# Optimization experiments

Hardware: AMD Instinct MI355X
Metric: run time of the kernel (lower is better)

## Reference

```python
import jax, jax.numpy as jnp
import numpy as np

B, N, D, S, ITERS, EPS = 32, 4096, 512, 8, 3, 1e-8


def layer_norm(x, g, b, eps=1e-5):
    mu = jnp.mean(x, axis=-1, keepdims=True)
    var = jnp.var(x, axis=-1, keepdims=True)
    return (x - mu) * jax.lax.rsqrt(var + eps) * g + b


def setup_inputs() -> dict:
    key = jax.random.key(0)
    ks = jax.random.split(key, 12)
    sc = 1.0 / np.sqrt(D)
    return {
        "inputs": jax.random.normal(ks[0], (B, N, D), jnp.float32),
        "noise": jax.random.normal(ks[1], (B, S, D), jnp.float32),
        "slots_mu": jax.random.normal(ks[2], (1, S, D), jnp.float32),
        "slots_sigma": jnp.ones((1, S, D), jnp.float32),
        "ln_in_g": jnp.ones((D,), jnp.float32), "ln_in_b": jnp.zeros((D,), jnp.float32),
        "ln_s_g": jnp.ones((D,), jnp.float32), "ln_s_b": jnp.zeros((D,), jnp.float32),
        "wq": jax.random.normal(ks[3], (D, D), jnp.float32) * sc,
        "wk": jax.random.normal(ks[4], (D, D), jnp.float32) * sc,
        "wv": jax.random.normal(ks[5], (D, D), jnp.float32) * sc,
        "w_ih": jax.random.normal(ks[6], (3 * D, D), jnp.float32) * sc,
        "w_hh": jax.random.normal(ks[7], (3 * D, D), jnp.float32) * sc,
        "b_ih": jnp.zeros((3 * D,), jnp.float32),
        "b_hh": jnp.zeros((3 * D,), jnp.float32),
        "ln_m_g": jnp.ones((D,), jnp.float32), "ln_m_b": jnp.zeros((D,), jnp.float32),
        "w1": jax.random.normal(ks[8], (D, D), jnp.float32) * sc,
        "b1": jnp.zeros((D,), jnp.float32),
        "w2": jax.random.normal(ks[9], (D, D), jnp.float32) * sc,
        "b2": jnp.zeros((D,), jnp.float32),
    }


def reference(inputs, noise, slots_mu, slots_sigma, ln_in_g, ln_in_b, ln_s_g, ln_s_b,
              wq, wk, wv, w_ih, w_hh, b_ih, b_hh, ln_m_g, ln_m_b, w1, b1, w2, b2):
    # slot init: mu + sigma * N(0,1)
    slots = slots_mu + slots_sigma * noise          # (B,S,D)
    x = layer_norm(inputs, ln_in_g, ln_in_b)        # (B,N,D)
    k = jnp.einsum('bnd,ed->bne', x, wk)            # (B,N,D)
    v = jnp.einsum('bnd,ed->bne', x, wv)            # (B,N,D)
    for _ in range(ITERS):
        slots_prev = slots
        sn = layer_norm(slots, ln_s_g, ln_s_b)
        q = jnp.einsum('bsd,ed->bse', sn, wq)       # (B,S,D)
        logits = jnp.einsum('bnd,bsd->bns', k, q)   # (B,N,S)
        attn = jax.nn.softmax(logits, axis=-1) + EPS  # softmax over slots
        attn = attn / jnp.sum(attn, axis=-1, keepdims=True)
        attn_t = jnp.swapaxes(attn, -1, -2)         # (B,S,N)
        updates = jnp.einsum('bsn,bnd->bsd', attn_t, v)
        # GRUCell(input=updates, hidden=slots_prev)
        gi = jnp.einsum('bsd,ed->bse', updates, w_ih) + b_ih
        gh = jnp.einsum('bsd,ed->bse', slots_prev, w_hh) + b_hh
        gi_r, gi_z, gi_n = jnp.split(gi, 3, axis=-1)
        gh_r, gh_z, gh_n = jnp.split(gh, 3, axis=-1)
        r = jax.nn.sigmoid(gi_r + gh_r)
        z = jax.nn.sigmoid(gi_z + gh_z)
        n = jnp.tanh(gi_n + r * gh_n)
        slots = (1.0 - z) * n + z * slots_prev
        # residual MLP
        h = layer_norm(slots, ln_m_g, ln_m_b)
        h = jax.nn.relu(jnp.einsum('bsd,ed->bse', h, w1) + b1)
        slots = slots + jnp.einsum('bsd,ed->bse', h, w2) + b2
    return slots
```

## Files before the change

kernel.cpp:

```cpp
#include <hip/hip_runtime.h>

#define B_ 32
#define N_ 4096
#define D_ 512
#define S_ 8
#define ITERS_ 3

__device__ __forceinline__ float sigmoid_f(float x) {
    return 1.0f / (1.0f + __expf(-x));
}
__device__ __forceinline__ float tanh_f(float x) {
    float e = __expf(2.0f * x);
    return 1.0f - 2.0f / (e + 1.0f);
}

template<int WT, int LNA>
__device__ void gemm_body(const float* __restrict__ A, const float* __restrict__ W,
                          const float* __restrict__ bias, float* __restrict__ C,
                          int M, int N, int K, int bxi, int byi,
                          const float* __restrict__ stats,
                          const float* __restrict__ lng, const float* __restrict__ lnb,
                          float* smem) {
    float (*As)[68] = (float (*)[68])smem;
    float (*Ws)[36] = (float (*)[36])(smem + 64 * 68);
    int t  = threadIdx.x;
    int bm = byi * 64, bn = bxi * 32;
    int tm = t >> 4, tn = t & 15;
    float acc[4][2] = {{0.f,0.f},{0.f,0.f},{0.f,0.f},{0.f,0.f}};

    for (int kk = 0; kk < K; kk += 64) {
        __syncthreads();
        if (WT == 2) {
#pragma unroll
            for (int r = 0; r < 4; ++r) {
                int idx = t + r * 256;
                int k = idx >> 4, m4 = idx & 15;
                float4 a4 = *(const float4*)(A + (size_t)(kk + k) * M + bm + (m4 << 2));
                *(float4*)&As[k][m4 << 2] = a4;
            }
        } else {
#pragma unroll
            for (int r = 0; r < 4; ++r) {
                int flat = t * 4 + r * 1024;
                int m = flat >> 6, k = flat & 63;
                float4 a4 = *(const float4*)(A + (size_t)(bm + m) * K + kk + k);
                if (LNA) {
                    float mean = stats[(bm + m) * 2];
                    float rs   = stats[(bm + m) * 2 + 1];
                    float4 g4 = *(const float4*)(lng + kk + k);
                    float4 b4 = *(const float4*)(lnb + kk + k);
                    a4.x = fmaf((a4.x - mean) * rs, g4.x, b4.x);
                    a4.y = fmaf((a4.y - mean) * rs, g4.y, b4.y);
                    a4.z = fmaf((a4.z - mean) * rs, g4.z, b4.z);
                    a4.w = fmaf((a4.w - mean) * rs, g4.w, b4.w);
                }
                As[k + 0][m] = a4.x; As[k + 1][m] = a4.y;
                As[k + 2][m] = a4.z; As[k + 3][m] = a4.w;
            }
        }
        if (WT == 1) {
#pragma unroll
            for (int r = 0; r < 2; ++r) {
                int flat = t * 4 + r * 1024;
                int n = flat >> 6, k = flat & 63;
                float4 w4 = *(const float4*)(W + (size_t)(bn + n) * K + kk + k);
                Ws[k + 0][n] = w4.x; Ws[k + 1][n] = w4.y;
                Ws[k + 2][n] = w4.z; Ws[k + 3][n] = w4.w;
            }
        } else {
#pragma unroll
            for (int r = 0; r < 2; ++r) {
                int flat = t * 4 + r * 1024;
                int k = flat >> 5, n = flat & 31;
                float4 w4 = *(const float4*)(W + (size_t)(kk + k) * N + bn + n);
                *(float4*)&Ws[k][n] = w4;
            }
        }
        __syncthreads();
#pragma unroll
        for (int k = 0; k < 64; ++k) {
            float4 a = *(const float4*)&As[k][tm << 2];
            float2 w = *(const float2*)&Ws[k][tn << 1];
            acc[0][0] = fmaf(a.x, w.x, acc[0][0]); acc[0][1] = fmaf(a.x, w.y, acc[0][1]);
            acc[1][0] = fmaf(a.y, w.x, acc[1][0]); acc[1][1] = fmaf(a.y, w.y, acc[1][1]);
            acc[2][0] = fmaf(a.z, w.x, acc[2][0]); acc[2][1] = fmaf(a.z, w.y, acc[2][1]);
            acc[3][0] = fmaf(a.w, w.x, acc[3][0]); acc[3][1] = fmaf(a.w, w.y, acc[3][1]);
        }
    }
#pragma unroll
    for (int i = 0; i < 4; ++i) {
#pragma unroll
        for (int j = 0; j < 2; ++j) {
            int row = bm + (tm << 2) + i;
            int col = bn + (tn << 1) + j;
            float v = acc[i][j];
            if (bias) v += bias[col];
            C[(size_t)row * N + col] = v;
        }
    }
}

__device__ void init_body(const float* __restrict__ noise, const float* __restrict__ mu,
                          const float* __restrict__ sg, float* __restrict__ slots,
                          float* __restrict__ stats, int blk) {
    int wid = threadIdx.x >> 6, lane = threadIdx.x & 63;
    int row = blk * 4 + wid;
    const float4* nz = (const float4*)(noise + (size_t)row * D_);
    const float4* m4 = (const float4*)(mu + (size_t)(row & 7) * D_);
    const float4* s4 = (const float4*)(sg + (size_t)(row & 7) * D_);
    float4 v0 = nz[lane], v1 = nz[64 + lane];
    float4 a0 = m4[lane], a1 = m4[64 + lane];
    float4 c0 = s4[lane], c1 = s4[64 + lane];
    v0.x = fmaf(c0.x, v0.x, a0.x); v0.y = fmaf(c0.y, v0.y, a0.y);
    v0.z = fmaf(c0.z, v0.z, a0.z); v0.w = fmaf(c0.w, v0.w, a0.w);
    v1.x = fmaf(c1.x, v1.x, a1.x); v1.y = fmaf(c1.y, v1.y, a1.y);
    v1.z = fmaf(c1.z, v1.z, a1.z); v1.w = fmaf(c1.w, v1.w, a1.w);
    float4* o4 = (float4*)(slots + (size_t)row * D_);
    o4[lane] = v0; o4[64 + lane] = v1;
    float s1 = v0.x + v0.y + v0.z + v0.w + v1.x + v1.y + v1.z + v1.w;
    float s2 = v0.x*v0.x; s2 = fmaf(v0.y,v0.y,s2); s2 = fmaf(v0.z,v0.z,s2); s2 = fmaf(v0.w,v0.w,s2);
    s2 = fmaf(v1.x,v1.x,s2); s2 = fmaf(v1.y,v1.y,s2); s2 = fmaf(v1.z,v1.z,s2); s2 = fmaf(v1.w,v1.w,s2);
#pragma unroll
    for (int off = 32; off > 0; off >>= 1) {
        s1 += __shfl_xor(s1, off, 64);
        s2 += __shfl_xor(s2, off, 64);
    }
    if (lane == 0) {
        float mean = s1 * (1.0f / D_);
        float var  = s2 * (1.0f / D_) - mean * mean;
        stats[row * 2]     = mean;
        stats[row * 2 + 1] = rsqrtf(var + 1e-5f);
    }
}

__global__ __launch_bounds__(256) void k_pro(const float* __restrict__ wk, const float* __restrict__ wq,
                                             const float* __restrict__ w_ih, const float* __restrict__ wv,
                                             float* __restrict__ Mqk, float* __restrict__ Wiv,
                                             const float* __restrict__ noise, const float* __restrict__ mu,
                                             const float* __restrict__ sg, float* __restrict__ slots,
                                             float* __restrict__ stats) {
    __shared__ float smem[64 * 68 + 64 * 36];
    int blk = blockIdx.x;
    if (blk < 128) {
        gemm_body<2,0>(wk, wq, nullptr, Mqk, 512, 512, 512, blk & 15, blk >> 4,
                       nullptr, nullptr, nullptr, smem);
    } else if (blk < 512) {
        int t2 = blk - 128;
        gemm_body<0,0>(w_ih, wv, nullptr, Wiv, 1536, 512, 512, t2 & 15, t2 >> 4,
                       nullptr, nullptr, nullptr, smem);
    } else {
        init_body(noise, mu, sg, slots, stats, blk - 512);
    }
}

template<int WT, int LNA>
__global__ __launch_bounds__(256) void k_gemm(const float* __restrict__ A, const float* __restrict__ W,
                                              const float* __restrict__ bias, float* __restrict__ C,
                                              int M, int N, int K,
                                              const float* __restrict__ stats,
                                              const float* __restrict__ lng, const float* __restrict__ lnb) {
    __shared__ float smem[64 * 68 + 64 * 36];
    gemm_body<WT,LNA>(A, W, bias, C, M, N, K, blockIdx.x, blockIdx.y, stats, lng, lnb, smem);
}

template<int FIRST>
__global__ __launch_bounds__(512, 1) void k_attn_gh(const float* __restrict__ x,
                                                    const float* __restrict__ qk,
                                                    const float* __restrict__ g,
                                                    const float* __restrict__ bvec,
                                                    float* __restrict__ part,
                                                    float* __restrict__ bsum,
                                                    float2* __restrict__ murs,
                                                    const float* __restrict__ slots,
                                                    const float* __restrict__ w_hh,
                                                    const float* __restrict__ b_hh,
                                                    float* __restrict__ gg) {
    __shared__ float smem[8704];
    const int blk = blockIdx.x;
    const int t = threadIdx.x;

    if (blk < 96) {
        const int ci = blk % 24, ri = blk / 24;
        const int bm = ri * 64, bn = ci * 64;
        float (*As)[68] = (float (*)[68])smem;
        float (*Ws)[68] = (float (*)[68])(smem + 64 * 68);
        const int tm = t >> 5, tn = t & 31;
        float acc[4][2] = {{0.f,0.f},{0.f,0.f},{0.f,0.f},{0.f,0.f}};
        for (int kk = 0; kk < 512; kk += 64) {
            __syncthreads();
#pragma unroll
            for (int r = 0; r < 2; ++r) {
                int flat = t * 4 + r * 2048;
                int m = flat >> 6, k = flat & 63;
                float4 a4 = *(const float4*)(slots + (size_t)(bm + m) * 512 + kk + k);
                As[k + 0][m] = a4.x; As[k + 1][m] = a4.y;
                As[k + 2][m] = a4.z; As[k + 3][m] = a4.w;
            }
#pragma unroll
            for (int r = 0; r < 2; ++r) {
                int flat = t * 4 + r * 2048;
                int n = flat >> 6, k = flat & 63;
                float4 w4 = *(const float4*)(w_hh + (size_t)(bn + n) * 512 + kk + k);
                Ws[k + 0][n] = w4.x; Ws[k + 1][n] = w4.y;
                Ws[k + 2][n] = w4.z; Ws[k + 3][n] = w4.w;
            }
            __syncthreads();
#pragma unroll
            for (int k = 0; k < 64; ++k) {
                const float4 a = *(const float4*)&As[k][tm << 2];
                const float2 w = *(const float2*)&Ws[k][tn << 1];
                acc[0][0] = fmaf(a.x, w.x, acc[0][0]); acc[0][1] = fmaf(a.x, w.y, acc[0][1]);
                acc[1][0] = fmaf(a.y, w.x, acc[1][0]); acc[1][1] = fmaf(a.y, w.y, acc[1][1]);
                acc[2][0] = fmaf(a.z, w.x, acc[2][0]); acc[2][1] = fmaf(a.z, w.y, acc[2][1]);
                acc[3][0] = fmaf(a.w, w.x, acc[3][0]); acc[3][1] = fmaf(a.w, w.y, acc[3][1]);
            }
        }
#pragma unroll
        for (int i = 0; i < 4; ++i) {
#pragma unroll
            for (int j = 0; j < 2; ++j) {
                int row = bm + (tm << 2) + i;
                int col = bn + (tn << 1) + j;
                gg[(size_t)row * 3072 + col] = acc[i][j] + b_hh[col];
            }
        }
        return;
    }

    float* qts  = smem;
    float* dds  = smem + 4096;
    float* wls  = smem + 4480;
    float* mur  = smem + 4864;
    float* redA = smem + 5376;
    float* redB = smem + 5392;
    float* c12  = smem + 5408;
    float* u0s  = smem;
    const int ablk = blk - 96;
    const int nc = ablk & 15, b = ablk >> 4;
    const int w = t >> 6, lane = t & 63;
    const size_t rowbase = (size_t)b * N_ + (size_t)nc * 256;

    {
        const float4* qk4 = (const float4*)(qk + (size_t)b * 4096);
        const float4* g4 = (const float4*)g;
        const float4* b4 = (const float4*)bvec;
        float c1p[2], c2p[2];
#pragma unroll
        for (int r = 0; r < 2; ++r) {
            int f = t + r * 512;
            int k4 = f & 127, sidx = f >> 7;
            float4 v = qk4[f];
            float4 gg4 = g4[k4];
            float4 bb = b4[k4];
            float4 qv = make_float4(v.x*gg4.x, v.y*gg4.y, v.z*gg4.z, v.w*gg4.w);
            *(float4*)&qts[(k4 * 8 + (sidx ^ (k4 & 7))) * 4] = qv;
            c1p[r] = qv.x + qv.y + qv.z + qv.w;
            c2p[r] = bb.x*v.x + bb.y*v.y + bb.z*v.z + bb.w*v.w;
        }
#pragma unroll
        for (int off = 32; off > 0; off >>= 1) {
#pragma unroll
            for (int r = 0; r < 2; ++r) {
                c1p[r] += __shfl_xor(c1p[r], off, 64);
                c2p[r] += __shfl_xor(c2p[r], off, 64);
            }
        }
        if (lane == 0) {
            redA[w * 2 + 0] = c1p[0]; redA[w * 2 + 1] = c1p[1];
            redB[w * 2 + 0] = c2p[0]; redB[w * 2 + 1] = c2p[1];
        }
    }
    if (!FIRST && t < 256) {
        float2 mm = murs[rowbase + t];
        mur[2 * t] = mm.x; mur[2 * t + 1] = mm.y;
    }
    __syncthreads();
    if (t < 8) {
        int s = t;
        float v1, v2;
        if (s < 4) { v1 = redA[4*s]       + redA[4*s + 2];     v2 = redB[4*s]       + redB[4*s + 2]; }
        else       { v1 = redA[4*(s-4)+1] + redA[4*(s-4)+3];   v2 = redB[4*(s-4)+1] + redB[4*(s-4)+3]; }
        c12[s] = v1; c12[8 + s] = v2;
    }
    __syncthreads();

    float4 qa[8], qb[8];
#pragma unroll
    for (int s = 0; s < 8; ++s) {
        qa[s] = *(const float4*)&qts[(lane * 8 + (s ^ (lane & 7))) * 4];
        qb[s] = *(const float4*)&qts[((64 + lane) * 8 + (s ^ (lane & 7))) * 4];
    }

    const bool hb5 = (lane & 32) != 0, hb4 = (lane & 16) != 0, hb3 = (lane & 8) != 0;
    const float cnorm = 1.0f / (1.0f + 8.0f * 1e-8f);
    const float eadd  = 1e-8f * cnorm;

    float4 acc0[8], acc1[8];
#pragma unroll
    for (int s = 0; s < 8; ++s) {
        acc0[s] = make_float4(0.f, 0.f, 0.f, 0.f);
        acc1[s] = make_float4(0.f, 0.f, 0.f, 0.f);
    }
    float aS8[8] = {0,0,0,0,0,0,0,0}, tS8[8] = {0,0,0,0,0,0,0,0};

    const float4* xg = (const float4*)(x + rowbase * D_);
    float4 cur[8], nxt[8];
    {
        int r0 = w * 4;
#pragma unroll
        for (int i = 0; i < 4; ++i) {
            cur[2*i]   = xg[(size_t)(r0 + i) * 128 + lane];
            cur[2*i+1] = xg[(size_t)(r0 + i) * 128 + 64 + lane];
        }
    }

    for (int jb = 0; jb < 8; ++jb) {
#pragma unroll
        for (int i = 0; i < 4; ++i) {
            float4 xa = cur[2*i], xb = cur[2*i+1];
            float dd[8];
#pragma unroll
            for (int s = 0; s < 8; ++s) {
                float td = xa.x * qa[s].x;
                td = fmaf(xa.y, qa[s].y, td); td = fmaf(xa.z, qa[s].z, td); td = fmaf(xa.w, qa[s].w, td);
                td = fmaf(xb.x, qb[s].x, td); td = fmaf(xb.y, qb[s].y, td);
                td = fmaf(xb.z, qb[s].z, td); td = fmaf(xb.w, qb[s].w, td);
                dd[s] = td;
            }
            float r4[4];
#pragma unroll
            for (int s = 0; s < 4; ++s) {
                float snd = hb5 ? dd[s] : dd[s + 4];
                float kp  = hb5 ? dd[s + 4] : dd[s];
                r4[s] = kp + __shfl_xor(snd, 32, 64);
            }
            float r2v[2];
#pragma unroll
            for (int s = 0; s < 2; ++s) {
                float snd = hb4 ? r4[s] : r4[s + 2];
                float kp  = hb4 ? r4[s + 2] : r4[s];
                r2v[s] = kp + __shfl_xor(snd, 16, 64);
            }
            float v;
            {
                float snd = hb3 ? r2v[0] : r2v[1];
                float kp  = hb3 ? r2v[1] : r2v[0];
                v = kp + __shfl_xor(snd, 8, 64);
            }
            v += __shfl_xor(v, 4, 64);
            v += __shfl_xor(v, 2, 64);
            v += __shfl_xor(v, 1, 64);
            int rb = w * 4 + i;
            if ((lane & 7) == 0) dds[rb * 12 + (lane >> 3)] = v;

            if (FIRST) {
                float sx = xa.x + xa.y + xa.z + xa.w + xb.x + xb.y + xb.z + xb.w;
                float sxx = xa.x*xa.x; sxx = fmaf(xa.y,xa.y,sxx); sxx = fmaf(xa.z,xa.z,sxx); sxx = fmaf(xa.w,xa.w,sxx);
                sxx = fmaf(xb.x,xb.x,sxx); sxx = fmaf(xb.y,xb.y,sxx); sxx = fmaf(xb.z,xb.z,sxx); sxx = fmaf(xb.w,xb.w,sxx);
#pragma unroll
                for (int off = 32; off > 0; off >>= 1) {
                    sx  += __shfl_xor(sx, off, 64);
                    sxx += __shfl_xor(sxx, off, 64);
                }
                float mean = sx * (1.0f / D_);
                float rs   = rsqrtf(sxx * (1.0f / D_) - mean * mean + 1e-5f);
                if (lane == 0) {
                    int br = jb * 32 + rb;
                    mur[br * 2] = mean; mur[br * 2 + 1] = rs;
                    murs[rowbase + br] = make_float2(mean, rs);
                }
            }
        }
        __syncthreads();
        if (w == 0 && lane < 32) {
            int br = jb * 32 + lane;
            float4 d03 = *(const float4*)&dds[lane * 12];
            float4 d47 = *(const float4*)&dds[lane * 12 + 4];
            float mean = mur[br * 2], rs = mur[br * 2 + 1];
            float mc = -rs * mean;
            float lg[8];
            lg[0] = fmaf(rs, d03.x, fmaf(mc, c12[0], c12[8]));
            lg[1] = fmaf(rs, d03.y, fmaf(mc, c12[1], c12[9]));
            lg[2] = fmaf(rs, d03.z, fmaf(mc, c12[2], c12[10]));
            lg[3] = fmaf(rs, d03.w, fmaf(mc, c12[3], c12[11]));
            lg[4] = fmaf(rs, d47.x, fmaf(mc, c12[4], c12[12]));
            lg[5] = fmaf(rs, d47.y, fmaf(mc, c12[5], c12[13]));
            lg[6] = fmaf(rs, d47.z, fmaf(mc, c12[6], c12[14]));
            lg[7] = fmaf(rs, d47.w, fmaf(mc, c12[7], c12[15]));
            float mx = lg[0];
#pragma unroll
            for (int s = 1; s < 8; ++s) mx = fmaxf(mx, lg[s]);
            float p[8], psum = 0.f;
#pragma unroll
            for (int s = 0; s < 8; ++s) { p[s] = __expf(lg[s] - mx); psum += p[s]; }
            float ip = cnorm / psum;
            float wv[8];
#pragma unroll
            for (int s = 0; s < 8; ++s) {
                float a = fmaf(p[s], ip, eadd);
                wv[s] = a * rs;
                aS8[s] += a;
                tS8[s] = fmaf(wv[s], mean, tS8[s]);
            }
            *(float4*)&wls[lane * 12]     = make_float4(wv[0], wv[1], wv[2], wv[3]);
            *(float4*)&wls[lane * 12 + 4] = make_float4(wv[4], wv[5], wv[6], wv[7]);
        }
        __syncthreads();
        {
            int jn = (jb < 7) ? jb + 1 : 7;
            int r0 = jn * 32 + w * 4;
#pragma unroll
            for (int i = 0; i < 4; ++i) {
                nxt[2*i]   = xg[(size_t)(r0 + i) * 128 + lane];
                nxt[2*i+1] = xg[(size_t)(r0 + i) * 128 + 64 + lane];
            }
        }
#pragma unroll
        for (int i = 0; i < 4; ++i) {
            int rb = w * 4 + i;
            float4 w03 = *(const float4*)&wls[rb * 12];
            float4 w47 = *(const float4*)&wls[rb * 12 + 4];
            float4 xa = cur[2*i], xb = cur[2*i+1];
            acc0[0].x = fmaf(w03.x, xa.x, acc0[0].x); acc0[0].y = fmaf(w03.x, xa.y, acc0[0].y);
            acc0[0].z = fmaf(w03.x, xa.z, acc0[0].z); acc0[0].w = fmaf(w03.x, xa.w, acc0[0].w);
            acc1[0].x = fmaf(w03.x, xb.x, acc1[0].x); acc1[0].y = fmaf(w03.x, xb.y, acc1[0].y);
            acc1[0].z = fmaf(w03.x, xb.z, acc1[0].z); acc1[0].w = fmaf(w03.x, xb.w, acc1[0].w);
            acc0[1].x = fmaf(w03.y, xa.x, acc0[1].x); acc0[1].y = fmaf(w03.y, xa.y, acc0[1].y);
            acc0[1].z = fmaf(w03.y, xa.z, acc0[1].z); acc0[1].w = fmaf(w03.y, xa.w, acc0[1].w);
            acc1[1].x = fmaf(w03.y, xb.x, acc1[1].x); acc1[1].y = fmaf(w03.y, xb.y, acc1[1].y);
            acc1[1].z = fmaf(w03.y, xb.z, acc1[1].z); acc1[1].w = fmaf(w03.y, xb.w, acc1[1].w);
            acc0[2].x = fmaf(w03.z, xa.x, acc0[2].x); acc0[2].y = fmaf(w03.z, xa.y, acc0[2].y);
            acc0[2].z = fmaf(w03.z, xa.z, acc0[2].z); acc0[2].w = fmaf(w03.z, xa.w, acc0[2].w);
            acc1[2].x = fmaf(w03.z, xb.x, acc1[2].x); acc1[2].y = fmaf(w03.z, xb.y, acc1[2].y);
            acc1[2].z = fmaf(w03.z, xb.z, acc1[2].z); acc1[2].w = fmaf(w03.z, xb.w, acc1[2].w);
            acc0[3].x = fmaf(w03.w, xa.x, acc0[3].x); acc0[3].y = fmaf(w03.w, xa.y, acc0[3].y);
            acc0[3].z = fmaf(w03.w, xa.z, acc0[3].z); acc0[3].w = fmaf(w03.w, xa.w, acc0[3].w);
            acc1[3].x = fmaf(w03.w, xb.x, acc1[3].x); acc1[3].y = fmaf(w03.w, xb.y, acc1[3].y);
            acc1[3].z = fmaf(w03.w, xb.z, acc1[3].z); acc1[3].w = fmaf(w03.w, xb.w, acc1[3].w);
            acc0[4].x = fmaf(w47.x, xa.x, acc0[4].x); acc0[4].y = fmaf(w47.x, xa.y, acc0[4].y);
            acc0[4].z = fmaf(w47.x, xa.z, acc0[4].z); acc0[4].w = fmaf(w47.x, xa.w, acc0[4].w);
            acc1[4].x = fmaf(w47.x, xb.x, acc1[4].x); acc1[4].y = fmaf(w47.x, xb.y, acc1[4].y);
            acc1[4].z = fmaf(w47.x, xb.z, acc1[4].z); acc1[4].w = fmaf(w47.x, xb.w, acc1[4].w);
            acc0[5].x = fmaf(w47.y, xa.x, acc0[5].x); acc0[5].y = fmaf(w47.y, xa.y, acc0[5].y);
            acc0[5].z = fmaf(w47.y, xa.z, acc0[5].z); acc0[5].w = fmaf(w47.y, xa.w, acc0[5].w);
            acc1[5].x = fmaf(w47.y, xb.x, acc1[5].x); acc1[5].y = fmaf(w47.y, xb.y, acc1[5].y);
            acc1[5].z = fmaf(w47.y, xb.z, acc1[5].z); acc1[5].w = fmaf(w47.y, xb.w, acc1[5].w);
            acc0[6].x = fmaf(w47.z, xa.x, acc0[6].x); acc0[6].y = fmaf(w47.z, xa.y, acc0[6].y);
            acc0[6].z = fmaf(w47.z, xa.z, acc0[6].z); acc0[6].w = fmaf(w47.z, xa.w, acc0[6].w);
            acc1[6].x = fmaf(w47.z, xb.x, acc1[6].x); acc1[6].y = fmaf(w47.z, xb.y, acc1[6].y);
            acc1[6].z = fmaf(w47.z, xb.z, acc1[6].z); acc1[6].w = fmaf(w47.z, xb.w, acc1[6].w);
            acc0[7].x = fmaf(w47.w, xa.x, acc0[7].x); acc0[7].y = fmaf(w47.w, xa.y, acc0[7].y);
            acc0[7].z = fmaf(w47.w, xa.z, acc0[7].z); acc0[7].w = fmaf(w47.w, xa.w, acc0[7].w);
            acc1[7].x = fmaf(w47.w, xb.x, acc1[7].x); acc1[7].y = fmaf(w47.w, xb.y, acc1[7].y);
            acc1[7].z = fmaf(w47.w, xb.z, acc1[7].z); acc1[7].w = fmaf(w47.w, xb.w, acc1[7].w);
        }
#pragma unroll
        for (int i = 0; i < 8; ++i) cur[i] = nxt[i];
        __syncthreads();
    }

    if (w == 0) {
#pragma unroll
        for (int off = 32; off > 0; off >>= 1) {
#pragma unroll
            for (int s = 0; s < 8; ++s) {
                aS8[s] += __shfl_xor(aS8[s], off, 64);
                tS8[s] += __shfl_xor(tS8[s], off, 64);
            }
        }
        if (lane == 0) {
            float* bs = bsum + (size_t)(b * 16 + nc) * 16;
#pragma unroll
            for (int s = 0; s < 8; ++s) { bs[s] = aS8[s]; bs[8 + s] = tS8[s]; }
        }
    }
    for (int w2 = 0; w2 < 8; ++w2) {
        if (w == w2) {
#pragma unroll
            for (int s = 0; s < 8; ++s) {
                float* p0 = &u0s[s * 512 + (lane << 2)];
                float* p1 = p0 + 256;
                if (w2 == 0) {
                    *(float4*)p0 = acc0[s];
                    *(float4*)p1 = acc1[s];
                } else {
                    float4 v0 = *(float4*)p0;
                    v0.x += acc0[s].x; v0.y += acc0[s].y; v0.z += acc0[s].z; v0.w += acc0[s].w;
                    *(float4*)p0 = v0;
                    float4 v1 = *(float4*)p1;
                    v1.x += acc1[s].x; v1.y += acc1[s].y; v1.z += acc1[s].z; v1.w += acc1[s].w;
                    *(float4*)p1 = v1;
                }
            }
        }
        __syncthreads();
    }
    float4* d4 = (float4*)(part + (size_t)(b * 16 + nc) * 4096);
    const float4* s4 = (const float4*)u0s;
    d4[t] = s4[t];
    d4[t + 512] = s4[t + 512];
}

__global__ __launch_bounds__(512) void k_ured(const float* __restrict__ part,
                                              const float* __restrict__ bsum,
                                              const float* __restrict__ g,
                                              const float* __restrict__ bvec,
                                              float* __restrict__ u0) {
    const int bs = blockIdx.x;
    const int b = bs >> 3, s = bs & 7;
    const int d = threadIdx.x;
    float Av = 0.f, Tv = 0.f;
#pragma unroll
    for (int nc = 0; nc < 16; ++nc) {
        Av += bsum[(size_t)(b * 16 + nc) * 16 + s];
        Tv += bsum[(size_t)(b * 16 + nc) * 16 + 8 + s];
    }
    float p = 0.f;
#pragma unroll
    for (int nc = 0; nc < 16; ++nc)
        p += part[(size_t)(b * 16 + nc) * 4096 + s * 512 + d];
    u0[(size_t)bs * 512 + d] = fmaf(g[d], p - Tv, Av * bvec[d]);
}

__global__ __launch_bounds__(256) void k_gi(const float* __restrict__ u0,
                                            const float* __restrict__ Wiv,
                                            const float* __restrict__ b_ih,
                                            float* __restrict__ gg) {
    __shared__ float As[64][68];
    __shared__ float Ws[64][36];
    const int t = threadIdx.x;
    const int bn = blockIdx.x * 32;
    const int bm = blockIdx.y * 64;
    int tm = t >> 4, tn = t & 15;
    float acc[4][2] = {{0.f,0.f},{0.f,0.f},{0.f,0.f},{0.f,0.f}};

    for (int kk = 0; kk < 512; kk += 64) {
        __syncthreads();
#pragma unroll
        for (int r = 0; r < 4; ++r) {
            int flat = t * 4 + r * 1024;
            int m = flat >> 6, k = flat & 63;
            float4 a4 = *(const float4*)(u0 + (size_t)(bm + m) * 512 + kk + k);
            As[k + 0][m] = a4.x; As[k + 1][m] = a4.y;
            As[k + 2][m] = a4.z; As[k + 3][m] = a4.w;
        }
#pragma unroll
        for (int r = 0; r < 2; ++r) {
            int flat = t * 4 + r * 1024;
            int n = flat >> 6, k = flat & 63;
            float4 w4 = *(const float4*)(Wiv + (size_t)(bn + n) * 512 + kk + k);
            Ws[k + 0][n] = w4.x; Ws[k + 1][n] = w4.y;
            Ws[k + 2][n] = w4.z; Ws[k + 3][n] = w4.w;
        }
        __syncthreads();
#pragma unroll
        for (int k = 0; k < 64; ++k) {
            float4 a = *(const float4*)&As[k][tm << 2];
            float2 w = *(const float2*)&Ws[k][tn << 1];
            acc[0][0] = fmaf(a.x, w.x, acc[0][0]); acc[0][1] = fmaf(a.x, w.y, acc[0][1]);
            acc[1][0] = fmaf(a.y, w.x, acc[1][0]); acc[1][1] = fmaf(a.y, w.y, acc[1][1]);
            acc[2][0] = fmaf(a.z, w.x, acc[2][0]); acc[2][1] = fmaf(a.z, w.y, acc[2][1]);
            acc[3][0] = fmaf(a.w, w.x, acc[3][0]); acc[3][1] = fmaf(a.w, w.y, acc[3][1]);
        }
    }
#pragma unroll
    for (int i = 0; i < 4; ++i) {
#pragma unroll
        for (int j = 0; j < 2; ++j) {
            int row = bm + (tm << 2) + i;
            int cw  = bn + (tn << 1) + j;
            gg[(size_t)row * 3072 + 1536 + cw] = acc[i][j] + b_ih[cw];
        }
    }
}

__global__ __launch_bounds__(512) void k_p2(const float* __restrict__ gg,
                                            const float* __restrict__ slots,
                                            const float* __restrict__ w1, const float* __restrict__ b1,
                                            const float* __restrict__ w2, const float* __restrict__ b2,
                                            const float* __restrict__ wqkT,
                                            const float* __restrict__ ln_m_g, const float* __restrict__ ln_m_b,
                                            const float* __restrict__ ln_s_g, const float* __restrict__ ln_s_b,
                                            float* __restrict__ dst, float* __restrict__ qkout, int last) {
    __shared__ float s2s[2][512];
    __shared__ float t0s[2][512];
    __shared__ float hs[2][512];
    __shared__ float stat[4];
    const int t = threadIdx.x;
    const int wid = t >> 6, lane = t & 63;
    const int r0 = blockIdx.x * 2;

#pragma unroll
    for (int j = 0; j < 2; ++j) {
        int flat = t + j * 512;
        int r = flat >> 9, d = flat & 511;
        size_t row = r0 + r;
        const float* ghb = gg + row * 3072;
        const float* gib = ghb + 1536;
        float gir = gib[d], giz = gib[d + 512], gin = gib[d + 1024];
        float ghr = ghb[d], ghz = ghb[d + 512], ghn = ghb[d + 1024];
        float rr = sigmoid_f(gir + ghr);
        float zz = sigmoid_f(giz + ghz);
        float nn = tanh_f(fmaf(rr, ghn, gin));
        float sp = slots[row * 512 + d];
        s2s[r][d] = fmaf(1.0f - zz, nn, zz * sp);
    }
    __syncthreads();
    if (wid < 2) {
        const float4* sr = (const float4*)s2s[wid];
        float4 a = sr[lane], bq = sr[64 + lane];
        float s1 = a.x + a.y + a.z + a.w + bq.x + bq.y + bq.z + bq.w;
        float s2 = a.x*a.x; s2 = fmaf(a.y,a.y,s2); s2 = fmaf(a.z,a.z,s2); s2 = fmaf(a.w,a.w,s2);
        s2 = fmaf(bq.x,bq.x,s2); s2 = fmaf(bq.y,bq.y,s2); s2 = fmaf(bq.z,bq.z,s2); s2 = fmaf(bq.w,bq.w,s2);
#pragma unroll
        for (int off = 32; off > 0; off >>= 1) {
            s1 += __shfl_xor(s1, off, 64);
            s2 += __shfl_xor(s2, off, 64);
        }
        if (lane == 0) {
            float mean = s1 * (1.0f / D_);
            float var  = s2 * (1.0f / D_) - mean * mean;
            stat[wid * 2] = mean;
            stat[wid * 2 + 1] = rsqrtf(var + 1e-5f);
        }
    }
    __syncthreads();
#pragma unroll
    for (int j = 0; j < 2; ++j) {
        int flat = t + j * 512;
        int r = flat >> 9, d = flat & 511;
        t0s[r][d] = fmaf((s2s[r][d] - stat[r * 2]) * stat[r * 2 + 1], ln_m_g[d], ln_m_b[d]);
    }
    __syncthreads();
    {
        const int c = t;
        const float4* wr = (const float4*)(w1 + (size_t)c * 512);
        float a0 = 0.f, a1 = 0.f;
#pragma unroll 8
        for (int k4 = 0; k4 < 128; ++k4) {
            float4 w4 = wr[k4];
            float4 q0 = *(const float4*)&t0s[0][k4 << 2];
            float4 q1 = *(const float4*)&t0s[1][k4 << 2];
            a0 = fmaf(q0.x, w4.x, a0); a0 = fmaf(q0.y, w4.y, a0);
            a0 = fmaf(q0.z, w4.z, a0); a0 = fmaf(q0.w, w4.w, a0);
            a1 = fmaf(q1.x, w4.x, a1); a1 = fmaf(q1.y, w4.y, a1);
            a1 = fmaf(q1.z, w4.z, a1); a1 = fmaf(q1.w, w4.w, a1);
        }
        float bc = b1[c];
        hs[0][c] = fmaxf(a0 + bc, 0.f);
        hs[1][c] = fmaxf(a1 + bc, 0.f);
    }
    __syncthreads();
    {
        const int c = t;
        const float4* wr = (const float4*)(w2 + (size_t)c * 512);
        float a0 = 0.f, a1 = 0.f;
#pragma unroll 8
        for (int k4 = 0; k4 < 128; ++k4) {
            float4 w4 = wr[k4];
            float4 q0 = *(const float4*)&hs[0][k4 << 2];
            float4 q1 = *(const float4*)&hs[1][k4 << 2];
            a0 = fmaf(q0.x, w4.x, a0); a0 = fmaf(q0.y, w4.y, a0);
            a0 = fmaf(q0.z, w4.z, a0); a0 = fmaf(q0.w, w4.w, a0);
            a1 = fmaf(q1.x, w4.x, a1); a1 = fmaf(q1.y, w4.y, a1);
            a1 = fmaf(q1.z, w4.z, a1); a1 = fmaf(q1.w, w4.w, a1);
        }
        float bc = b2[c];
        float o0 = s2s[0][c] + a0 + bc;
        float o1 = s2s[1][c] + a1 + bc;
        dst[(size_t)r0 * 512 + c] = o0;
        dst[(size_t)(r0 + 1) * 512 + c] = o1;
        s2s[0][c] = o0;
        s2s[1][c] = o1;
    }
    if (last) return;
    __syncthreads();
    if (wid < 2) {
        const float4* sr = (const float4*)s2s[wid];
        float4 a = sr[lane], bq = sr[64 + lane];
        float s1 = a.x + a.y + a.z + a.w + bq.x + bq.y + bq.z + bq.w;
        float s2 = a.x*a.x; s2 = fmaf(a.y,a.y,s2); s2 = fmaf(a.z,a.z,s2); s2 = fmaf(a.w,a.w,s2);
        s2 = fmaf(bq.x,bq.x,s2); s2 = fmaf(bq.y,bq.y,s2); s2 = fmaf(bq.z,bq.z,s2); s2 = fmaf(bq.w,bq.w,s2);
#pragma unroll
        for (int off = 32; off > 0; off >>= 1) {
            s1 += __shfl_xor(s1, off, 64);
            s2 += __shfl_xor(s2, off, 64);
        }
        if (lane == 0) {
            float mean = s1 * (1.0f / D_);
            float var  = s2 * (1.0f / D_) - mean * mean;
            stat[wid * 2] = mean;
            stat[wid * 2 + 1] = rsqrtf(var + 1e-5f);
        }
    }
    __syncthreads();
#pragma unroll
    for (int j = 0; j < 2; ++j) {
        int flat = t + j * 512;
        int r = flat >> 9, d = flat & 511;
        t0s[r][d] = fmaf((s2s[r][d] - stat[r * 2]) * stat[r * 2 + 1], ln_s_g[d], ln_s_b[d]);
    }
    __syncthreads();
    {
        const int c = t;
        const float4* wr = (const float4*)(wqkT + (size_t)c * 512);
        float a0 = 0.f, a1 = 0.f;
#pragma unroll 8
        for (int k4 = 0; k4 < 128; ++k4) {
            float4 w4 = wr[k4];
            float4 q0 = *(const float4*)&t0s[0][k4 << 2];
            float4 q1 = *(const float4*)&t0s[1][k4 << 2];
            a0 = fmaf(q0.x, w4.x, a0); a0 = fmaf(q0.y, w4.y, a0);
            a0 = fmaf(q0.z, w4.z, a0); a0 = fmaf(q0.w, w4.w, a0);
            a1 = fmaf(q1.x, w4.x, a1); a1 = fmaf(q1.y, w4.y, a1);
            a1 = fmaf(q1.z, w4.z, a1); a1 = fmaf(q1.w, w4.w, a1);
        }
        qkout[(size_t)r0 * 512 + c] = a0;
        qkout[(size_t)(r0 + 1) * 512 + c] = a1;
    }
}

extern "C" void kernel_launch(void* const* d_in, const int* in_sizes, int n_in,
                              void* d_out, int out_size, void* d_ws, size_t ws_size,
                              hipStream_t stream) {
    const float* inputs  = (const float*)d_in[0];
    const float* noise   = (const float*)d_in[1];
    const float* mu      = (const float*)d_in[2];
    const float* sg      = (const float*)d_in[3];
    const float* ln_in_g = (const float*)d_in[4];
    const float* ln_in_b = (const float*)d_in[5];
    const float* ln_s_g  = (const float*)d_in[6];
    const float* ln_s_b  = (const float*)d_in[7];
    const float* wq      = (const float*)d_in[8];
    const float* wk      = (const float*)d_in[9];
    const float* wv      = (const float*)d_in[10];
    const float* w_ih    = (const float*)d_in[11];
    const float* w_hh    = (const float*)d_in[12];
    const float* b_ih    = (const float*)d_in[13];
    const float* b_hh    = (const float*)d_in[14];
    const float* ln_m_g  = (const float*)d_in[15];
    const float* ln_m_b  = (const float*)d_in[16];
    const float* w1      = (const float*)d_in[17];
    const float* b1      = (const float*)d_in[18];
    const float* w2      = (const float*)d_in[19];
    const float* b2      = (const float*)d_in[20];

    float* ws = (float*)d_ws;
    const size_t SLOT = (size_t)B_ * S_ * D_;
    size_t o = 0;
    float* slots = ws + o; o += SLOT;
    float* qk    = ws + o; o += SLOT;
    float* u0    = ws + o; o += SLOT;
    float* gg    = ws + o; o += (size_t)256 * 3072;
    float* Mqk   = ws + o; o += (size_t)D_ * D_;
    float* Wiv   = ws + o; o += (size_t)3 * D_ * D_;
    float* statsS= ws + o; o += 512;
    float* part  = ws + o; o += (size_t)16 * B_ * 4096;
    float* bsum  = ws + o; o += (size_t)B_ * 16 * 16;
    float2* murs = (float2*)(ws + o); o += (size_t)2 * B_ * N_;

    k_pro<<<576, 256, 0, stream>>>(wk, wq, w_ih, wv, Mqk, Wiv, noise, mu, sg, slots, statsS);
    k_gemm<1,1><<<dim3(16, 4), 256, 0, stream>>>(slots, Mqk, nullptr, qk,
                                                 256, 512, 512, statsS, ln_s_g, ln_s_b);

    for (int it = 0; it < ITERS_; ++it) {
        if (it == 0)
            k_attn_gh<1><<<608, 512, 0, stream>>>(inputs, qk, ln_in_g, ln_in_b, part, bsum,
                                                  murs, slots, w_hh, b_hh, gg);
        else
            k_attn_gh<0><<<608, 512, 0, stream>>>(inputs, qk, ln_in_g, ln_in_b, part, bsum,
                                                  murs, slots, w_hh, b_hh, gg);
        k_ured<<<256, 512, 0, stream>>>(part, bsum, ln_in_g, ln_in_b, u0);
        k_gi<<<dim3(48, 4), 256, 0, stream>>>(u0, Wiv, b_ih, gg);
        int last = (it == ITERS_ - 1);
        float* dst = last ? (float*)d_out : slots;
        k_p2<<<128, 512, 0, stream>>>(gg, slots, w1, b1, w2, b2, Mqk,
                                      ln_m_g, ln_m_b, ln_s_g, ln_s_b, dst, qk, last);
    }
}
```

Before: 677.0 us.

## Double attention rows per block and distribute softmax per wave to drop barriers

Each attention block now covers 512 rows instead of 256, halving the number of attention blocks and the partial buffers that k_ured must reduce. The per-chunk softmax is computed by four lanes in each wave for that wave's own rows instead of by wave 0 after a block barrier, which removes two __syncthreads per chunk. The prefetch of the next x chunk moves to the top of the loop. Per-block slot sums are reduced through shared memory across waves. In exchange, fewer blocks may lower occupancy and load balance across CUs, and the shared-memory layout changes.

```diff
diff --git a/kernel.cpp b/kernel.cpp
--- a/kernel.cpp
+++ b/kernel.cpp
@@ -231,14 +231,14 @@
     float* dds  = smem + 4096;
     float* wls  = smem + 4480;
     float* mur  = smem + 4864;
-    float* redA = smem + 5376;
-    float* redB = smem + 5392;
-    float* c12  = smem + 5408;
+    float* redA = smem + 5888;
+    float* redB = smem + 5952;
+    float* c12  = smem + 6016;
     float* u0s  = smem;
     const int ablk = blk - 96;
-    const int nc = ablk & 15, b = ablk >> 4;
+    const int nc = ablk & 7, b = ablk >> 3;
     const int w = t >> 6, lane = t & 63;
-    const size_t rowbase = (size_t)b * N_ + (size_t)nc * 256;
+    const size_t rowbase = (size_t)b * N_ + (size_t)nc * 512;
 
     {
         const float4* qk4 = (const float4*)(qk + (size_t)b * 4096);
@@ -270,7 +270,7 @@
             redB[w * 2 + 0] = c2p[0]; redB[w * 2 + 1] = c2p[1];
         }
     }
-    if (!FIRST && t < 256) {
+    if (!FIRST) {
         float2 mm = murs[rowbase + t];
         mur[2 * t] = mm.x; mur[2 * t + 1] = mm.y;
     }
@@ -314,7 +314,16 @@
         }
     }
 
-    for (int jb = 0; jb < 8; ++jb) {
+    for (int jb = 0; jb < 16; ++jb) {
+        {
+            int jn = (jb < 15) ? jb + 1 : 15;
+            int r0 = jn * 32 + w * 4;
+#pragma unroll
+            for (int i = 0; i < 4; ++i) {
+                nxt[2*i]   = xg[(size_t)(r0 + i) * 128 + lane];
+                nxt[2*i+1] = xg[(size_t)(r0 + i) * 128 + 64 + lane];
+            }
+        }
 #pragma unroll
         for (int i = 0; i < 4; ++i) {
             float4 xa = cur[2*i], xb = cur[2*i+1];
@@ -371,11 +380,11 @@
                 }
             }
         }
-        __syncthreads();
-        if (w == 0 && lane < 32) {
-            int br = jb * 32 + lane;
-            float4 d03 = *(const float4*)&dds[lane * 12];
-            float4 d47 = *(const float4*)&dds[lane * 12 + 4];
+        if (lane < 4) {
+            int rb = w * 4 + lane;
+            int br = jb * 32 + rb;
+            float4 d03 = *(const float4*)&dds[rb * 12];
+            float4 d47 = *(const float4*)&dds[rb * 12 + 4];
             float mean = mur[br * 2], rs = mur[br * 2 + 1];
             float mc = -rs * mean;
             float lg[8];
@@ -402,18 +411,8 @@
                 aS8[s] += a;
                 tS8[s] = fmaf(wv[s], mean, tS8[s]);
             }
-            *(float4*)&wls[lane * 12]     = make_float4(wv[0], wv[1], wv[2], wv[3]);
-            *(float4*)&wls[lane * 12 + 4] = make_float4(wv[4], wv[5], wv[6], wv[7]);
-        }
-        __syncthreads();
-        {
-            int jn = (jb < 7) ? jb + 1 : 7;
-            int r0 = jn * 32 + w * 4;
-#pragma unroll
-            for (int i = 0; i < 4; ++i) {
-                nxt[2*i]   = xg[(size_t)(r0 + i) * 128 + lane];
-                nxt[2*i+1] = xg[(size_t)(r0 + i) * 128 + 64 + lane];
-            }
+            *(float4*)&wls[rb * 12]     = make_float4(wv[0], wv[1], wv[2], wv[3]);
+            *(float4*)&wls[rb * 12 + 4] = make_float4(wv[4], wv[5], wv[6], wv[7]);
         }
 #pragma unroll
         for (int i = 0; i < 4; ++i) {
@@ -456,23 +455,18 @@
         }
 #pragma unroll
         for (int i = 0; i < 8; ++i) cur[i] = nxt[i];
-        __syncthreads();
-    }
-
-    if (w == 0) {
-#pragma unroll
-        for (int off = 32; off > 0; off >>= 1) {
-#pragma unroll
-            for (int s = 0; s < 8; ++s) {
-                aS8[s] += __shfl_xor(aS8[s], off, 64);
-                tS8[s] += __shfl_xor(tS8[s], off, 64);
-            }
-        }
-        if (lane == 0) {
-            float* bs = bsum + (size_t)(b * 16 + nc) * 16;
-#pragma unroll
-            for (int s = 0; s < 8; ++s) { bs[s] = aS8[s]; bs[8 + s] = tS8[s]; }
-        }
+    }
+
+#pragma unroll
+    for (int s = 0; s < 8; ++s) {
+        aS8[s] += __shfl_xor(aS8[s], 1, 64);
+        aS8[s] += __shfl_xor(aS8[s], 2, 64);
+        tS8[s] += __shfl_xor(tS8[s], 1, 64);
+        tS8[s] += __shfl_xor(tS8[s], 2, 64);
+    }
+    if (lane == 0) {
+#pragma unroll
+        for (int s = 0; s < 8; ++s) { redA[w * 8 + s] = aS8[s]; redB[w * 8 + s] = tS8[s]; }
     }
     for (int w2 = 0; w2 < 8; ++w2) {
         if (w == w2) {
@@ -495,7 +489,15 @@
         }
         __syncthreads();
     }
-    float4* d4 = (float4*)(part + (size_t)(b * 16 + nc) * 4096);
+    if (t < 16) {
+        int s = t & 7;
+        const float* src = (t < 8) ? redA : redB;
+        float v = 0.f;
+#pragma unroll
+        for (int w2 = 0; w2 < 8; ++w2) v += src[w2 * 8 + s];
+        bsum[(size_t)(b * 8 + nc) * 16 + t] = v;
+    }
+    float4* d4 = (float4*)(part + (size_t)(b * 8 + nc) * 4096);
     const float4* s4 = (const float4*)u0s;
     d4[t] = s4[t];
     d4[t + 512] = s4[t + 512];
@@ -511,14 +513,14 @@
     const int d = threadIdx.x;
     float Av = 0.f, Tv = 0.f;
 #pragma unroll
-    for (int nc = 0; nc < 16; ++nc) {
-        Av += bsum[(size_t)(b * 16 + nc) * 16 + s];
-        Tv += bsum[(size_t)(b * 16 + nc) * 16 + 8 + s];
+    for (int nc = 0; nc < 8; ++nc) {
+        Av += bsum[(size_t)(b * 8 + nc) * 16 + s];
+        Tv += bsum[(size_t)(b * 8 + nc) * 16 + 8 + s];
     }
     float p = 0.f;
 #pragma unroll
-    for (int nc = 0; nc < 16; ++nc)
-        p += part[(size_t)(b * 16 + nc) * 4096 + s * 512 + d];
+    for (int nc = 0; nc < 8; ++nc)
+        p += part[(size_t)(b * 8 + nc) * 4096 + s * 512 + d];
     u0[(size_t)bs * 512 + d] = fmaf(g[d], p - Tv, Av * bvec[d]);
 }
 
@@ -755,8 +757,8 @@
     float* Mqk   = ws + o; o += (size_t)D_ * D_;
     float* Wiv   = ws + o; o += (size_t)3 * D_ * D_;
     float* statsS= ws + o; o += 512;
-    float* part  = ws + o; o += (size_t)16 * B_ * 4096;
-    float* bsum  = ws + o; o += (size_t)B_ * 16 * 16;
+    float* part  = ws + o; o += (size_t)8 * B_ * 4096;
+    float* bsum  = ws + o; o += (size_t)B_ * 8 * 16;
     float2* murs = (float2*)(ws + o); o += (size_t)2 * B_ * N_;
 
     k_pro<<<576, 256, 0, stream>>>(wk, wq, w_ih, wv, Mqk, Wiv, noise, mu, sg, slots, statsS);
@@ -765,10 +767,10 @@
 
     for (int it = 0; it < ITERS_; ++it) {
         if (it == 0)
-            k_attn_gh<1><<<608, 512, 0, stream>>>(inputs, qk, ln_in_g, ln_in_b, part, bsum,
+            k_attn_gh<1><<<352, 512, 0, stream>>>(inputs, qk, ln_in_g, ln_in_b, part, bsum,
                                                   murs, slots, w_hh, b_hh, gg);
         else
-            k_attn_gh<0><<<608, 512, 0, stream>>>(inputs, qk, ln_in_g, ln_in_b, part, bsum,
+            k_attn_gh<0><<<352, 512, 0, stream>>>(inputs, qk, ln_in_g, ln_in_b, part, bsum,
                                                   murs, slots, w_hh, b_hh, gg);
         k_ured<<<256, 512, 0, stream>>>(part, bsum, ln_in_g, ln_in_b, u0);
         k_gi<<<dim3(48, 4), 256, 0, stream>>>(u0, Wiv, b_ih, gg);
```

After: 664.6 us. No clear change (-1.8%).
